# Performance work log

Measured on AMD Instinct MI355X. Metric: run time of the kernel, lower is better.

Reference implementation:

```python
import jax, jax.numpy as jnp
import numpy as np

NEG = -1e30  # stand-in for -inf on the H-attention diagonal (matches INF helper)


def _conv1x1(w, b, x):
    # w: [O, C], x: [B, C, H, W]
    return jnp.einsum('oc,bchw->bohw', w, x) + b[None, :, None, None]


def _cc_attn(q, k, v):
    """Criss-cross attention: q,k [B,Cq,H,W], v [B,C,H,W] -> [B,C,H,W]."""
    B, _, H, W = q.shape
    # column (H) energies: query at (h,w) attends to keys at (h', w)
    eH = jnp.einsum('bchw,bcjw->bhwj', q, k)  # [B,H,W,H]
    eye = jnp.eye(H, dtype=bool)[None, :, None, :]
    eH = jnp.where(eye, NEG, eH)  # mask h==h' (self counted once via W pass)
    # row (W) energies: query at (h,w) attends to keys at (h, w')
    eW = jnp.einsum('bchw,bchj->bhwj', q, k)  # [B,H,W,W]
    att = jax.nn.softmax(jnp.concatenate([eH, eW], axis=3), axis=3)  # [B,H,W,H+W]
    aH, aW = att[..., :H], att[..., H:]
    outH = jnp.einsum('bhwj,bcjw->bchw', aH, v)
    outW = jnp.einsum('bhwj,bchj->bchw', aW, v)
    return outH + outW


def setup_inputs() -> dict:
    key = jax.random.key(0)
    ks = jax.random.split(key, 14)
    B, C, H, W = 8, 256, 96, 96
    Cq = C // 8
    n = jax.random.normal
    return {
        'x': n(ks[0], (B, C, H, W), jnp.float32),
        'y': n(ks[1], (B, C, H, W), jnp.float32),
        'Wq': n(ks[2], (Cq, C), jnp.float32) * 0.05,
        'bq': n(ks[3], (Cq,), jnp.float32) * 0.05,
        'Wk': n(ks[4], (Cq, C), jnp.float32) * 0.05,
        'bk': n(ks[5], (Cq,), jnp.float32) * 0.05,
        'Wv': n(ks[6], (C, C), jnp.float32) * 0.05,
        'bv': n(ks[7], (C,), jnp.float32) * 0.05,
        'gamma1': n(ks[8], (1,), jnp.float32) * 0.1,
        'gamma2': n(ks[9], (1,), jnp.float32) * 0.1,
        'Wd': n(ks[10], (2 * C, 1, 3, 3), jnp.float32) * 0.1,  # depthwise, groups=2C
        'bd': n(ks[11], (2 * C,), jnp.float32) * 0.05,
        'Wp': n(ks[12], (C, 2 * C), jnp.float32) * 0.05,  # pointwise 1x1
        'bp': n(ks[13], (C,), jnp.float32) * 0.05,
    }


def reference(x, y, Wq, bq, Wk, bk, Wv, bv, gamma1, gamma2, Wd, bd, Wp, bp):
    qx = _conv1x1(Wq, bq, x)
    kx = _conv1x1(Wk, bk, x)
    vx = _conv1x1(Wv, bv, x)
    qy = _conv1x1(Wq, bq, y)
    ky = _conv1x1(Wk, bk, y)
    vy = _conv1x1(Wv, bv, y)
    # pass 1: attention weights from x, values from y
    out1 = gamma1[0] * _cc_attn(qx, kx, vy) + x
    # pass 2: attention weights from y, values from x
    out2 = gamma2[0] * _cc_attn(qy, ky, vx) + y
    z = jnp.concatenate([out1, out2], axis=1)  # [B, 2C, H, W]
    # depthwise 3x3 (groups = 2C), padding 1
    z = jax.lax.conv_general_dilated(
        z, Wd, window_strides=(1, 1), padding='SAME',
        feature_group_count=z.shape[1],
        dimension_numbers=('NCHW', 'OIHW', 'NCHW')) + bd[None, :, None, None]
    # pointwise 1x1 then LeakyReLU (torch default negative_slope=0.01)
    z = _conv1x1(Wp, bp, z)
    return jax.nn.leaky_relu(z, negative_slope=0.01)
```

## Files before the change

### kernel.cpp

```cpp
#include <hip/hip_runtime.h>
#include <hip/hip_bf16.h>

constexpr int kB  = 8;
constexpr int kC  = 256;
constexpr int kCq = 32;
constexpr int kH  = 96;
constexpr int kW  = 96;
constexpr int kP  = kH * kW;

using bf16x8 = __attribute__((ext_vector_type(8))) short;
using bf16x4 = __attribute__((ext_vector_type(4))) short;
using f32x4  = __attribute__((ext_vector_type(4))) float;

__device__ inline bf16x8 ld_lds8(const __hip_bfloat16* p) {
    bf16x4 lo = *(const bf16x4*)p;
    bf16x4 hi = *(const bf16x4*)(p + 4);
    return __builtin_shufflevector(lo, hi, 0, 1, 2, 3, 4, 5, 6, 7);
}

__device__ inline void async_copy16(const void* g, void* l) {
    __builtin_amdgcn_global_load_lds(
        (const __attribute__((address_space(1))) unsigned int*)g,
        (__attribute__((address_space(3))) unsigned int*)l, 16, 0, 0);
}

__global__ __launch_bounds__(256) void w_convert(
    const float* __restrict__ Wq, const float* __restrict__ Wk,
    const float* __restrict__ Wv,
    __hip_bfloat16* __restrict__ Wqkb, __hip_bfloat16* __restrict__ Wvb)
{
    const int i = blockIdx.x * 256 + threadIdx.x;
    if (i < 8192)       Wqkb[i] = __float2bfloat16(Wq[i]);
    else if (i < 16384) Wqkb[i] = __float2bfloat16(Wk[i - 8192]);
    else                Wvb[i - 16384] = __float2bfloat16(Wv[i - 16384]);
}

__global__ __launch_bounds__(256, 2) void qkv_mfma(
    const float* __restrict__ in_qk, const float* __restrict__ in_v,
    const __hip_bfloat16* __restrict__ Wqkb, const __hip_bfloat16* __restrict__ Wvb,
    const float* __restrict__ bq, const float* __restrict__ bk,
    const float* __restrict__ bv,
    __hip_bfloat16* __restrict__ Qbh, __hip_bfloat16* __restrict__ Qbl,
    __hip_bfloat16* __restrict__ Kbh, __hip_bfloat16* __restrict__ Kbl,
    __hip_bfloat16* __restrict__ Vpm, __hip_bfloat16* __restrict__ Vhw)
{
    __shared__ __align__(16) char smem[34816];
    float* stg = (float*)smem;
    __hip_bfloat16* vt = (__hip_bfloat16*)smem;

    const int b = blockIdx.y, t = threadIdx.x;
    const int wv = t >> 6, l = t & 63;
    const int n = l & 15, q = l >> 4;
    const int p0 = blockIdx.x * 64;
    const int p  = p0 + wv * 16 + n;
    const size_t bP = (size_t)b * kP;

    const float* __restrict__ xq = in_qk + (size_t)b * kC * kP + p0;
    const float* __restrict__ xv = in_v  + (size_t)b * kC * kP + p0;

    f32x4 acc[20];
#pragma unroll
    for (int i = 0; i < 20; i++) acc[i] = (f32x4)0.f;

    const int lrow = l >> 4, lpx = (l & 15) * 4;
#define STAGE_CHUNK(kc, buf)                                                   \
    {                                                                          \
        const size_t cb = (size_t)(kc) * 32;                                   \
        float* dq = stg + (size_t)(buf) * 4096;                                \
        float* dv = dq + 2048;                                                 \
        _Pragma("unroll")                                                      \
        for (int j = 0; j < 2; j++) {                                          \
            const int r0 = wv * 8 + j * 4;                                     \
            async_copy16(&xq[(cb + r0 + lrow) * kP + lpx], &dq[r0 * 64]);      \
            async_copy16(&xv[(cb + r0 + lrow) * kP + lpx], &dv[r0 * 64]);      \
        }                                                                      \
    }

    STAGE_CHUNK(0, 0);
    __syncthreads();

    int cur = 0;
    for (int kc = 0; kc < 8; kc++) {
        if (kc < 7) STAGE_CHUNK(kc + 1, cur ^ 1);

        const int c0 = kc * 32 + q * 8;

        bf16x8 wq[4], wv2[16];
#pragma unroll
        for (int mt = 0; mt < 4; mt++)
            wq[mt] = *(const bf16x8*)(Wqkb + ((mt * 16 + n) << 8) + c0);
#pragma unroll
        for (int mt = 0; mt < 16; mt++)
            wv2[mt] = *(const bf16x8*)(Wvb + ((mt * 16 + n) << 8) + c0);

        const float* __restrict__ sqf = stg + (size_t)cur * 4096;
        const float* __restrict__ svf = sqf + 2048;
        const int pl = wv * 16 + n;
        union { bf16x8 v; __hip_bfloat16 h[8]; } bfq, bfv;
#pragma unroll
        for (int j = 0; j < 8; j++)
            bfq.h[j] = __float2bfloat16(sqf[(q * 8 + j) * 64 + pl]);
#pragma unroll
        for (int j = 0; j < 8; j++)
            bfv.h[j] = __float2bfloat16(svf[(q * 8 + j) * 64 + pl]);

#pragma unroll
        for (int mt = 0; mt < 4; mt++)
            acc[mt] = __builtin_amdgcn_mfma_f32_16x16x32_bf16(wq[mt], bfq.v, acc[mt], 0, 0, 0);
#pragma unroll
        for (int mt = 0; mt < 16; mt++)
            acc[4 + mt] = __builtin_amdgcn_mfma_f32_16x16x32_bf16(wv2[mt], bfv.v, acc[4 + mt], 0, 0, 0);

        __syncthreads();
        cur ^= 1;
    }
#undef STAGE_CHUNK

#pragma unroll
    for (int mt = 0; mt < 2; mt++) {
        float4 bias = *(const float4*)&bq[mt * 16 + q * 4];
        float vv[4] = { acc[mt][0] + bias.x, acc[mt][1] + bias.y,
                        acc[mt][2] + bias.z, acc[mt][3] + bias.w };
        union { ushort4 u; __hip_bfloat16 h[4]; } hi, lo;
#pragma unroll
        for (int r = 0; r < 4; r++) {
            __hip_bfloat16 h = __float2bfloat16(vv[r]);
            hi.h[r] = h;
            lo.h[r] = __float2bfloat16(vv[r] - __bfloat162float(h));
        }
        *(ushort4*)&Qbh[(bP + p) * kCq + mt * 16 + q * 4] = hi.u;
        *(ushort4*)&Qbl[(bP + p) * kCq + mt * 16 + q * 4] = lo.u;
    }
#pragma unroll
    for (int mt = 2; mt < 4; mt++) {
        float4 bias = *(const float4*)&bk[(mt - 2) * 16 + q * 4];
        float vv[4] = { acc[mt][0] + bias.x, acc[mt][1] + bias.y,
                        acc[mt][2] + bias.z, acc[mt][3] + bias.w };
        union { ushort4 u; __hip_bfloat16 h[4]; } hi, lo;
#pragma unroll
        for (int r = 0; r < 4; r++) {
            __hip_bfloat16 h = __float2bfloat16(vv[r]);
            hi.h[r] = h;
            lo.h[r] = __float2bfloat16(vv[r] - __bfloat162float(h));
        }
        *(ushort4*)&Kbh[(bP + p) * kCq + (mt - 2) * 16 + q * 4] = hi.u;
        *(ushort4*)&Kbl[(bP + p) * kCq + (mt - 2) * 16 + q * 4] = lo.u;
    }

#pragma unroll
    for (int mt = 0; mt < 16; mt++) {
        float4 bias = *(const float4*)&bv[mt * 16 + q * 4];
        float vv[4] = { acc[4 + mt][0] + bias.x, acc[4 + mt][1] + bias.y,
                        acc[4 + mt][2] + bias.z, acc[4 + mt][3] + bias.w };
        union { ushort4 u; __hip_bfloat16 h[4]; } pm;
#pragma unroll
        for (int r = 0; r < 4; r++) pm.h[r] = __float2bfloat16(vv[r]);
        *(ushort4*)&Vpm[(bP + p) * kC + mt * 16 + q * 4] = pm.u;
#pragma unroll
        for (int r = 0; r < 4; r++)
            vt[(mt * 16 + q * 4 + r) * 68 + wv * 16 + n] = pm.h[r];
    }
    __syncthreads();

    {
        __hip_bfloat16* dst = Vhw + ((size_t)b * kC + t) * kP + p0;
#pragma unroll
        for (int j = 0; j < 8; j++) {
            bf16x8 row = ld_lds8(&vt[t * 68 + j * 8]);
            *(bf16x8*)&dst[j * 8] = row;
        }
    }
}

__global__ __launch_bounds__(256) void cc_stats(
    const __hip_bfloat16* __restrict__ Qbh, const __hip_bfloat16* __restrict__ Qbl,
    const __hip_bfloat16* __restrict__ Kbh, const __hip_bfloat16* __restrict__ Kbl,
    float* __restrict__ Sm, float* __restrict__ Si)
{
    __shared__ __align__(16) __hip_bfloat16 QH[96][36], QLo[96][36];
    __shared__ __align__(16) __hip_bfloat16 KH[96][36], KLo[96][36];
    __shared__ __align__(16) float EL[96][97];
    const int w = blockIdx.x, b = blockIdx.y;
    const int t = threadIdx.x;
    const size_t bP = (size_t)b * kP;

    for (int idx = t; idx < 768; idx += 256) {
        int row = idx >> 3, ch = (idx & 7) * 4;
        size_t g = (bP + (size_t)row * kW + w) * kCq + ch;
        *(ushort4*)&QH[row][ch]  = *(const ushort4*)&Qbh[g];
        *(ushort4*)&QLo[row][ch] = *(const ushort4*)&Qbl[g];
        *(ushort4*)&KH[row][ch]  = *(const ushort4*)&Kbh[g];
        *(ushort4*)&KLo[row][ch] = *(const ushort4*)&Kbl[g];
    }
    __syncthreads();

    const int wv = t >> 6, l = t & 63, ln = l & 15, lq = l >> 4;
#pragma unroll
    for (int s = 0; s < 9; s++) {
        int tile = wv * 9 + s, it = tile / 6, jt = tile % 6;
        bf16x8 ah = ld_lds8(&QH[it * 16 + ln][lq * 8]);
        bf16x8 al = ld_lds8(&QLo[it * 16 + ln][lq * 8]);
        bf16x8 bh = ld_lds8(&KH[jt * 16 + ln][lq * 8]);
        bf16x8 bl = ld_lds8(&KLo[jt * 16 + ln][lq * 8]);
        f32x4 d = (f32x4)0.f;
        d = __builtin_amdgcn_mfma_f32_16x16x32_bf16(al, bh, d, 0, 0, 0);
        d = __builtin_amdgcn_mfma_f32_16x16x32_bf16(ah, bl, d, 0, 0, 0);
        d = __builtin_amdgcn_mfma_f32_16x16x32_bf16(ah, bh, d, 0, 0, 0);
#pragma unroll
        for (int r = 0; r < 4; r++)
            EL[it * 16 + lq * 4 + r][jt * 16 + ln] = d[r];
    }
    __syncthreads();

    const int sub = t & 7;
    for (int pi = t >> 3; pi < 96; pi += 32) {
        float ev[12];
        float mx = -3.0e38f;
#pragma unroll
        for (int k = 0; k < 12; k++) {
            int j = sub + 8 * k;
            float e = EL[pi][j];
            if (j == pi) e = -3.0e38f;
            ev[k] = e;
            mx = fmaxf(mx, e);
        }
#pragma unroll
        for (int k = 1; k < 8; k <<= 1) mx = fmaxf(mx, __shfl_xor(mx, k, 8));
        float ss = 0.f;
#pragma unroll
        for (int k = 0; k < 12; k++) ss += __expf(ev[k] - mx);
#pragma unroll
        for (int k = 1; k < 8; k <<= 1) ss += __shfl_xor(ss, k, 8);
        if (sub == 0) {
            Sm[bP + (size_t)pi * kW + w] = mx;
            Si[bP + (size_t)pi * kW + w] = ss;
        }
    }
}

__global__ __launch_bounds__(256) void cc_pass1(
    const __hip_bfloat16* __restrict__ Qbh, const __hip_bfloat16* __restrict__ Qbl,
    const __hip_bfloat16* __restrict__ Kbh, const __hip_bfloat16* __restrict__ Kbl,
    const __hip_bfloat16* __restrict__ Vhw,
    const float* __restrict__ res_in, const float* __restrict__ gamma_p,
    __hip_bfloat16* __restrict__ Zb, float* __restrict__ Sm, float* __restrict__ Si,
    int s_off)
{
    __shared__ __align__(16) __hip_bfloat16 QH[32][36], QLo[32][36];
    __shared__ __align__(16) __hip_bfloat16 KH[96][36], KLo[96][36];
    __shared__ __align__(16) float EL[32][97];
    __shared__ __align__(16) __hip_bfloat16 attL[32][100];
    const int wt = blockIdx.x, h = blockIdx.y, b = blockIdx.z;
    const int w0 = wt * 32;
    const int t = threadIdx.x;
    const size_t bP = (size_t)b * kP;

    {
        int row = t >> 3, ch = (t & 7) * 4;
        size_t g = (bP + (size_t)h * kW + w0 + row) * kCq + ch;
        *(ushort4*)&QH[row][ch]  = *(const ushort4*)&Qbh[g];
        *(ushort4*)&QLo[row][ch] = *(const ushort4*)&Qbl[g];
    }
    for (int idx = t; idx < 768; idx += 256) {
        int row = idx >> 3, ch = (idx & 7) * 4;
        size_t g = (bP + (size_t)h * kW + row) * kCq + ch;
        *(ushort4*)&KH[row][ch]  = *(const ushort4*)&Kbh[g];
        *(ushort4*)&KLo[row][ch] = *(const ushort4*)&Kbl[g];
    }
    __syncthreads();

    const int wv = t >> 6, l = t & 63, ln = l & 15, lq = l >> 4;
#pragma unroll
    for (int s = 0; s < 3; s++) {
        int tile = wv * 3 + s, it = tile / 6, jt = tile % 6;
        bf16x8 ah = ld_lds8(&QH[it * 16 + ln][lq * 8]);
        bf16x8 al = ld_lds8(&QLo[it * 16 + ln][lq * 8]);
        bf16x8 bh = ld_lds8(&KH[jt * 16 + ln][lq * 8]);
        bf16x8 bl = ld_lds8(&KLo[jt * 16 + ln][lq * 8]);
        f32x4 d = (f32x4)0.f;
        d = __builtin_amdgcn_mfma_f32_16x16x32_bf16(al, bh, d, 0, 0, 0);
        d = __builtin_amdgcn_mfma_f32_16x16x32_bf16(ah, bl, d, 0, 0, 0);
        d = __builtin_amdgcn_mfma_f32_16x16x32_bf16(ah, bh, d, 0, 0, 0);
#pragma unroll
        for (int r = 0; r < 4; r++)
            EL[it * 16 + lq * 4 + r][jt * 16 + ln] = d[r];
    }
    __syncthreads();

    {
        const int pi = t >> 3, sub = t & 7;
        size_t sidx = bP + (size_t)h * kW + w0 + pi;
        float mH = Sm[sidx], sH = Si[sidx];
        float ev[12];
        float mx = mH;
#pragma unroll
        for (int k = 0; k < 12; k++) {
            float e = EL[pi][sub + 8 * k];
            ev[k] = e;
            mx = fmaxf(mx, e);
        }
#pragma unroll
        for (int k = 1; k < 8; k <<= 1) mx = fmaxf(mx, __shfl_xor(mx, k, 8));
        float ss = 0.f;
#pragma unroll
        for (int k = 0; k < 12; k++) { float e = __expf(ev[k] - mx); ev[k] = e; ss += e; }
#pragma unroll
        for (int k = 1; k < 8; k <<= 1) ss += __shfl_xor(ss, k, 8);
        float stot = ss + sH * __expf(mH - mx);
        float inv = 1.0f / stot;
        if (sub == 0) { Sm[sidx] = mx; Si[sidx] = inv; }
#pragma unroll
        for (int k = 0; k < 12; k++)
            attL[pi][sub + 8 * k] = __float2bfloat16(ev[k] * inv);
    }
    __syncthreads();

    const float* __restrict__ res = res_in + (size_t)b * kC * kP + (size_t)h * kW + w0;
    float4 rsv[4][2];
#pragma unroll
    for (int c4 = 0; c4 < 4; c4++) {
        const int c = (wv * 4 + c4) * 16 + ln;
#pragma unroll
        for (int it = 0; it < 2; it++)
            rsv[c4][it] = *(const float4*)&res[(size_t)c * kP + it * 16 + lq * 4];
    }

    bf16x8 aF[2][3];
#pragma unroll
    for (int it = 0; it < 2; it++)
#pragma unroll
        for (int j3 = 0; j3 < 3; j3++)
            aF[it][j3] = ld_lds8(&attL[it * 16 + ln][j3 * 32 + lq * 8]);

    f32x4 acc[2][4];
#pragma unroll
    for (int it = 0; it < 2; it++)
#pragma unroll
        for (int c4 = 0; c4 < 4; c4++) acc[it][c4] = (f32x4)0.f;

#pragma unroll
    for (int c4 = 0; c4 < 4; c4++) {
        const int c = (wv * 4 + c4) * 16 + ln;
        const __hip_bfloat16* vr = Vhw + ((size_t)b * kC + c) * kP + (size_t)h * kW;
        bf16x8 bF0 = *(const bf16x8*)&vr[lq * 8];
        bf16x8 bF1 = *(const bf16x8*)&vr[32 + lq * 8];
        bf16x8 bF2 = *(const bf16x8*)&vr[64 + lq * 8];
#pragma unroll
        for (int it = 0; it < 2; it++) {
            acc[it][c4] = __builtin_amdgcn_mfma_f32_16x16x32_bf16(aF[it][0], bF0, acc[it][c4], 0, 0, 0);
            acc[it][c4] = __builtin_amdgcn_mfma_f32_16x16x32_bf16(aF[it][1], bF1, acc[it][c4], 0, 0, 0);
            acc[it][c4] = __builtin_amdgcn_mfma_f32_16x16x32_bf16(aF[it][2], bF2, acc[it][c4], 0, 0, 0);
        }
    }

    const float gamma = gamma_p[0];
#pragma unroll
    for (int c4 = 0; c4 < 4; c4++) {
        const int c = (wv * 4 + c4) * 16 + ln;
#pragma unroll
        for (int it = 0; it < 2; it++) {
            const float* rp = (const float*)&rsv[c4][it];
#pragma unroll
            for (int r = 0; r < 4; r++) {
                int i = it * 16 + lq * 4 + r;
                float z = gamma * acc[it][c4][r] + rp[r];
                Zb[(bP + (size_t)h * kW + w0 + i) * 512 + s_off + c] = __float2bfloat16(z);
            }
        }
    }
}

__global__ __launch_bounds__(256) void cc_pass2(
    const __hip_bfloat16* __restrict__ Qbh, const __hip_bfloat16* __restrict__ Qbl,
    const __hip_bfloat16* __restrict__ Kbh, const __hip_bfloat16* __restrict__ Kbl,
    const __hip_bfloat16* __restrict__ Vpm,
    const float* __restrict__ gamma_p, __hip_bfloat16* __restrict__ Zb,
    const float* __restrict__ Sm, const float* __restrict__ Si, int s_off)
{
    __shared__ __align__(16) __hip_bfloat16 QH[32][36], QLo[32][36];
    __shared__ __align__(16) __hip_bfloat16 KH[96][36], KLo[96][36];
    __shared__ __align__(16) __hip_bfloat16 VL[96][260];
    __shared__ __align__(16) __hip_bfloat16 attL[32][100];
    const int ht = blockIdx.x, w = blockIdx.y, b = blockIdx.z;
    const int h0 = ht * 32;
    const int t = threadIdx.x;
    const size_t bP = (size_t)b * kP;

    {
        int row = t >> 3, ch = (t & 7) * 4;
        size_t g = (bP + (size_t)(h0 + row) * kW + w) * kCq + ch;
        *(ushort4*)&QH[row][ch]  = *(const ushort4*)&Qbh[g];
        *(ushort4*)&QLo[row][ch] = *(const ushort4*)&Qbl[g];
    }
    for (int idx = t; idx < 768; idx += 256) {
        int row = idx >> 3, ch = (idx & 7) * 4;
        size_t g = (bP + (size_t)row * kW + w) * kCq + ch;
        *(ushort4*)&KH[row][ch]  = *(const ushort4*)&Kbh[g];
        *(ushort4*)&KLo[row][ch] = *(const ushort4*)&Kbl[g];
    }
    for (int idx = t; idx < 96 * 32; idx += 256) {
        int j = idx >> 5, cg = (idx & 31) * 8;
        const ushort4* src = (const ushort4*)&Vpm[(bP + (size_t)j * kW + w) * kC + cg];
        ushort4 v0 = src[0], v1 = src[1];
        *(ushort4*)&VL[j][cg]     = v0;
        *(ushort4*)&VL[j][cg + 4] = v1;
    }
    __syncthreads();

    const int wv = t >> 6, l = t & 63, ln = l & 15, lq = l >> 4;
#pragma unroll
    for (int s = 0; s < 3; s++) {
        int tile = wv * 3 + s, it = tile / 6, jt = tile % 6;
        bf16x8 ah = ld_lds8(&QH[it * 16 + ln][lq * 8]);
        bf16x8 al = ld_lds8(&QLo[it * 16 + ln][lq * 8]);
        bf16x8 bh = ld_lds8(&KH[jt * 16 + ln][lq * 8]);
        bf16x8 bl = ld_lds8(&KLo[jt * 16 + ln][lq * 8]);
        f32x4 d = (f32x4)0.f;
        d = __builtin_amdgcn_mfma_f32_16x16x32_bf16(al, bh, d, 0, 0, 0);
        d = __builtin_amdgcn_mfma_f32_16x16x32_bf16(ah, bl, d, 0, 0, 0);
        d = __builtin_amdgcn_mfma_f32_16x16x32_bf16(ah, bh, d, 0, 0, 0);
        const int j = jt * 16 + ln;
#pragma unroll
        for (int r = 0; r < 4; r++) {
            int i = it * 16 + lq * 4 + r;
            size_t sidx = bP + (size_t)(h0 + i) * kW + w;
            float m = Sm[sidx], inv = Si[sidx];
            float a = (j == h0 + i) ? 0.f : __expf(d[r] - m) * inv;
            attL[i][j] = __float2bfloat16(a);
        }
    }
    __syncthreads();

    bf16x8 aF[2][3];
#pragma unroll
    for (int it = 0; it < 2; it++)
#pragma unroll
        for (int j3 = 0; j3 < 3; j3++)
            aF[it][j3] = ld_lds8(&attL[it * 16 + ln][j3 * 32 + lq * 8]);

    f32x4 acc[2][4];
#pragma unroll
    for (int it = 0; it < 2; it++)
#pragma unroll
        for (int c4 = 0; c4 < 4; c4++) acc[it][c4] = (f32x4)0.f;

#pragma unroll
    for (int c4 = 0; c4 < 4; c4++) {
        const int c = (wv * 4 + c4) * 16 + ln;
#pragma unroll
        for (int j3 = 0; j3 < 3; j3++) {
            union { bf16x8 v; __hip_bfloat16 h[8]; } bF;
#pragma unroll
            for (int jj = 0; jj < 8; jj++)
                bF.h[jj] = VL[j3 * 32 + lq * 8 + jj][c];
#pragma unroll
            for (int it = 0; it < 2; it++)
                acc[it][c4] = __builtin_amdgcn_mfma_f32_16x16x32_bf16(aF[it][j3], bF.v, acc[it][c4], 0, 0, 0);
        }
    }

    const float gamma = gamma_p[0];
#pragma unroll
    for (int c4 = 0; c4 < 4; c4++) {
        const int c = (wv * 4 + c4) * 16 + ln;
#pragma unroll
        for (int it = 0; it < 2; it++) {
#pragma unroll
            for (int r = 0; r < 4; r++) {
                int i = it * 16 + lq * 4 + r;
                size_t zi = (bP + (size_t)(h0 + i) * kW + w) * 512 + s_off + c;
                float old = __bfloat162float(Zb[zi]);
                Zb[zi] = __float2bfloat16(old + gamma * acc[it][c4][r]);
            }
        }
    }
}

__global__ __launch_bounds__(256) void wp_convert(
    const float* __restrict__ Wp, __hip_bfloat16* __restrict__ Wpb)
{
    const int i = blockIdx.x * 256 + threadIdx.x;
    Wpb[i] = __float2bfloat16(Wp[i]);
}

__global__ __launch_bounds__(256, 4) void dwpw(
    const __hip_bfloat16* __restrict__ Zb,
    const float* __restrict__ Wdw, const float* __restrict__ bd,
    const __hip_bfloat16* __restrict__ Wpb, const float* __restrict__ bp,
    float* __restrict__ out)
{
    __shared__ __align__(16) __hip_bfloat16 zs[16][520];

    const int wt = blockIdx.x, h = blockIdx.y, b = blockIdx.z;
    const int w0 = wt * 16;
    const int t = threadIdx.x;
    const size_t bP = (size_t)b * kP;

    const int l = t & 63, wv = t >> 6;
    const int lo16 = l & 15, q = l >> 4;

    const bf16x8* __restrict__ Bb[4];
#pragma unroll
    for (int nt = 0; nt < 4; nt++)
        Bb[nt] = (const bf16x8*)(Wpb + (size_t)(wv * 64 + nt * 16 + lo16) * 512);

    {
        float wd0[9], wd1[9];
#pragma unroll
        for (int k = 0; k < 9; k++) {
            wd0[k] = Wdw[(size_t)(2 * t) * 9 + k];
            wd1[k] = Wdw[(size_t)(2 * t + 1) * 9 + k];
        }
        const float b0 = bd[2 * t], b1 = bd[2 * t + 1];
        const uint* __restrict__ Zp = (const uint*)Zb + bP * 256 + t;
        const bool rvm = (h > 0), rvp = (h < kH - 1);

#pragma unroll
        for (int j0 = 0; j0 < 16; j0 += 8) {
            uint raw[10][3];
#pragma unroll
            for (int col = 0; col < 10; col++) {
                const int ww = w0 + j0 - 1 + col;
                const bool cv = (ww >= 0) && (ww < kW);
#pragma unroll
                for (int r = 0; r < 3; r++) {
                    const bool v = cv && (r == 1 || (r == 0 ? rvm : rvp));
                    raw[col][r] = v ? Zp[(size_t)((h + r - 1) * kW + ww) * 256] : 0u;
                }
            }
            float2 wfc[10][3];
#pragma unroll
            for (int col = 0; col < 10; col++)
#pragma unroll
                for (int r = 0; r < 3; r++) {
                    __hip_bfloat162 z2 = *(const __hip_bfloat162*)&raw[col][r];
                    wfc[col][r] = __bfloat1622float2(z2);
                }
#pragma unroll
            for (int j = 0; j < 8; j++) {
                float a0 = b0, a1 = b1;
#pragma unroll
                for (int r = 0; r < 3; r++) {
#pragma unroll
                    for (int dw = 0; dw < 3; dw++) {
                        const float2 z = wfc[j + dw][r];
                        const int k = r * 3 + dw;
                        a0 += wd0[k] * z.x;
                        a1 += wd1[k] * z.y;
                    }
                }
                __hip_bfloat162 pz;
                pz.x = __float2bfloat16(a0);
                pz.y = __float2bfloat16(a1);
                ((__hip_bfloat162*)&zs[j0 + j][0])[t] = pz;
            }
        }
    }

    bf16x8 wbuf[4][4];
#pragma unroll
    for (int kp = 0; kp < 4; kp++)
#pragma unroll
        for (int nt = 0; nt < 4; nt++)
            wbuf[kp][nt] = Bb[nt][kp * 4 + q];

    __syncthreads();

    f32x4 acc[4];
#pragma unroll
    for (int nt = 0; nt < 4; nt++) acc[nt] = (f32x4)0.f;

#pragma unroll
    for (int kc = 0; kc < 16; kc++) {
        const int s = kc & 3;
        bf16x8 a0 = ld_lds8(&zs[lo16][kc * 32 + q * 8]);
        bf16x8 wcur[4];
#pragma unroll
        for (int nt = 0; nt < 4; nt++) wcur[nt] = wbuf[s][nt];
        if (kc < 12) {
#pragma unroll
            for (int nt = 0; nt < 4; nt++)
                wbuf[s][nt] = Bb[nt][(kc + 4) * 4 + q];
        }
#pragma unroll
        for (int nt = 0; nt < 4; nt++)
            acc[nt] = __builtin_amdgcn_mfma_f32_16x16x32_bf16(a0, wcur[nt], acc[nt], 0, 0, 0);
    }

#pragma unroll
    for (int nt = 0; nt < 4; nt++) {
        const int ol = wv * 64 + nt * 16 + lo16;
        const float bias = bp[ol];
        float4 rv;
        float v0 = acc[nt][0] + bias; rv.x = v0 > 0.f ? v0 : 0.01f * v0;
        float v1 = acc[nt][1] + bias; rv.y = v1 > 0.f ? v1 : 0.01f * v1;
        float v2 = acc[nt][2] + bias; rv.z = v2 > 0.f ? v2 : 0.01f * v2;
        float v3 = acc[nt][3] + bias; rv.w = v3 > 0.f ? v3 : 0.01f * v3;
        *(float4*)&out[((size_t)b * 256 + ol) * kP + (size_t)h * kW + w0 + q * 4] = rv;
    }
}

extern "C" void kernel_launch(void* const* d_in, const int* in_sizes, int n_in,
                              void* d_out, int out_size, void* d_ws, size_t ws_size,
                              hipStream_t stream)
{
    const float* x   = (const float*)d_in[0];
    const float* y   = (const float*)d_in[1];
    const float* Wq  = (const float*)d_in[2];
    const float* bq  = (const float*)d_in[3];
    const float* Wk  = (const float*)d_in[4];
    const float* bk  = (const float*)d_in[5];
    const float* Wv  = (const float*)d_in[6];
    const float* bv  = (const float*)d_in[7];
    const float* g1  = (const float*)d_in[8];
    const float* g2  = (const float*)d_in[9];
    const float* Wdw = (const float*)d_in[10];
    const float* bd  = (const float*)d_in[11];
    const float* Wp  = (const float*)d_in[12];
    const float* bp  = (const float*)d_in[13];
    float* out = (float*)d_out;

    char* wsb = (char*)d_ws;
    __hip_bfloat16* Zb  = (__hip_bfloat16*)wsb;
    __hip_bfloat16* Qbh = (__hip_bfloat16*)(wsb + 75497472);
    __hip_bfloat16* Qbl = Qbh + 2359296;
    __hip_bfloat16* Kbh = (__hip_bfloat16*)(wsb + 84934656);
    __hip_bfloat16* Kbl = Kbh + 2359296;
    float* Sm = (float*)(wsb + 94371840);
    float* Si = (float*)(wsb + 94666752);
    __hip_bfloat16* Wqkb = (__hip_bfloat16*)Sm;
    __hip_bfloat16* Wvb  = ((__hip_bfloat16*)Sm) + 16384;
    __hip_bfloat16* Wpb  = (__hip_bfloat16*)(wsb + 75497472);
    __hip_bfloat16* Vpm  = (__hip_bfloat16*)d_out;
    __hip_bfloat16* Vhw  = Vpm + 18874368;

    hipLaunchKernelGGL(w_convert, dim3(320), dim3(256), 0, stream,
                       Wq, Wk, Wv, Wqkb, Wvb);
    hipLaunchKernelGGL(qkv_mfma, dim3(kP / 64, kB), dim3(256), 0, stream,
                       x, y, Wqkb, Wvb, bq, bk, bv, Qbh, Qbl, Kbh, Kbl, Vpm, Vhw);
    hipLaunchKernelGGL(cc_stats, dim3(kW, kB), dim3(256), 0, stream,
                       Qbh, Qbl, Kbh, Kbl, Sm, Si);
    hipLaunchKernelGGL(cc_pass1, dim3(kW / 32, kH, kB), dim3(256), 0, stream,
                       Qbh, Qbl, Kbh, Kbl, Vhw, x, g1, Zb, Sm, Si, 0);
    hipLaunchKernelGGL(cc_pass2, dim3(kH / 32, kW, kB), dim3(256), 0, stream,
                       Qbh, Qbl, Kbh, Kbl, Vpm, g1, Zb, Sm, Si, 0);
    hipLaunchKernelGGL(w_convert, dim3(320), dim3(256), 0, stream,
                       Wq, Wk, Wv, Wqkb, Wvb);
    hipLaunchKernelGGL(qkv_mfma, dim3(kP / 64, kB), dim3(256), 0, stream,
                       y, x, Wqkb, Wvb, bq, bk, bv, Qbh, Qbl, Kbh, Kbl, Vpm, Vhw);
    hipLaunchKernelGGL(cc_stats, dim3(kW, kB), dim3(256), 0, stream,
                       Qbh, Qbl, Kbh, Kbl, Sm, Si);
    hipLaunchKernelGGL(cc_pass1, dim3(kW / 32, kH, kB), dim3(256), 0, stream,
                       Qbh, Qbl, Kbh, Kbl, Vhw, y, g2, Zb, Sm, Si, 256);
    hipLaunchKernelGGL(cc_pass2, dim3(kH / 32, kW, kB), dim3(256), 0, stream,
                       Qbh, Qbl, Kbh, Kbl, Vpm, g2, Zb, Sm, Si, 256);
    hipLaunchKernelGGL(wp_convert, dim3(512), dim3(256), 0, stream, Wp, Wpb);
    hipLaunchKernelGGL(dwpw, dim3(kW / 16, kH, kB), dim3(256), 0, stream,
                       Zb, Wdw, bd, Wpb, bp, out);
}
```

Measured before the change: 816.3 us.

## Replace pixel-major V with column-transposed V layout for H-pass attention

Stops qkv_mfma from writing the pixel-major V copy and adds a small transpose kernel that builds a per-channel, column-major (w,h) copy of V from the existing [C,H,W] copy. cc_pass2 then loads its MFMA B-operands directly from global memory as contiguous 8-element vectors instead of staging a 96x256 V tile in LDS and gathering it with scalar strided reads. This removes a large LDS allocation and its fill loop, which may raise occupancy. In exchange it adds an extra kernel launch and a full read and write of V per pass.

```diff
diff --git a/kernel.cpp b/kernel.cpp
--- a/kernel.cpp
+++ b/kernel.cpp
@@ -42,7 +42,7 @@
     const float* __restrict__ bv,
     __hip_bfloat16* __restrict__ Qbh, __hip_bfloat16* __restrict__ Qbl,
     __hip_bfloat16* __restrict__ Kbh, __hip_bfloat16* __restrict__ Kbl,
-    __hip_bfloat16* __restrict__ Vpm, __hip_bfloat16* __restrict__ Vhw)
+    __hip_bfloat16* __restrict__ Vhw)
 {
     __shared__ __align__(16) char smem[34816];
     float* stg = (float*)smem;
@@ -152,13 +152,9 @@
         float4 bias = *(const float4*)&bv[mt * 16 + q * 4];
         float vv[4] = { acc[4 + mt][0] + bias.x, acc[4 + mt][1] + bias.y,
                         acc[4 + mt][2] + bias.z, acc[4 + mt][3] + bias.w };
-        union { ushort4 u; __hip_bfloat16 h[4]; } pm;
-#pragma unroll
-        for (int r = 0; r < 4; r++) pm.h[r] = __float2bfloat16(vv[r]);
-        *(ushort4*)&Vpm[(bP + p) * kC + mt * 16 + q * 4] = pm.u;
 #pragma unroll
         for (int r = 0; r < 4; r++)
-            vt[(mt * 16 + q * 4 + r) * 68 + wv * 16 + n] = pm.h[r];
+            vt[(mt * 16 + q * 4 + r) * 68 + wv * 16 + n] = __float2bfloat16(vv[r]);
     }
     __syncthreads();
 
@@ -169,6 +165,31 @@
             bf16x8 row = ld_lds8(&vt[t * 68 + j * 8]);
             *(bf16x8*)&dst[j * 8] = row;
         }
+    }
+}
+
+__global__ __launch_bounds__(256) void vcol_tr(
+    const __hip_bfloat16* __restrict__ Vhw, __hip_bfloat16* __restrict__ Vcol)
+{
+    __shared__ __hip_bfloat16 tile[96][105];
+    const int bc = blockIdx.x;
+    const size_t base = (size_t)bc * kP;
+    const int t = threadIdx.x;
+
+    for (int ci = t; ci < 1152; ci += 256) {
+        const int off = ci * 8, h = off / 96, w = off - h * 96;
+        union { bf16x8 v; __hip_bfloat16 e[8]; } in;
+        in.v = *(const bf16x8*)&Vhw[base + off];
+#pragma unroll
+        for (int j = 0; j < 8; j++) tile[h][w + j] = in.e[j];
+    }
+    __syncthreads();
+    for (int ci = t; ci < 1152; ci += 256) {
+        const int off = ci * 8, w = off / 96, h = off - w * 96;
+        union { bf16x8 v; __hip_bfloat16 e[8]; } o;
+#pragma unroll
+        for (int j = 0; j < 8; j++) o.e[j] = tile[h + j][w];
+        *(bf16x8*)&Vcol[base + off] = o.v;
     }
 }
 
@@ -373,13 +394,12 @@
 __global__ __launch_bounds__(256) void cc_pass2(
     const __hip_bfloat16* __restrict__ Qbh, const __hip_bfloat16* __restrict__ Qbl,
     const __hip_bfloat16* __restrict__ Kbh, const __hip_bfloat16* __restrict__ Kbl,
-    const __hip_bfloat16* __restrict__ Vpm,
+    const __hip_bfloat16* __restrict__ Vcol,
     const float* __restrict__ gamma_p, __hip_bfloat16* __restrict__ Zb,
     const float* __restrict__ Sm, const float* __restrict__ Si, int s_off)
 {
     __shared__ __align__(16) __hip_bfloat16 QH[32][36], QLo[32][36];
     __shared__ __align__(16) __hip_bfloat16 KH[96][36], KLo[96][36];
-    __shared__ __align__(16) __hip_bfloat16 VL[96][260];
     __shared__ __align__(16) __hip_bfloat16 attL[32][100];
     const int ht = blockIdx.x, w = blockIdx.y, b = blockIdx.z;
     const int h0 = ht * 32;
@@ -397,13 +417,6 @@
         size_t g = (bP + (size_t)row * kW + w) * kCq + ch;
         *(ushort4*)&KH[row][ch]  = *(const ushort4*)&Kbh[g];
         *(ushort4*)&KLo[row][ch] = *(const ushort4*)&Kbl[g];
-    }
-    for (int idx = t; idx < 96 * 32; idx += 256) {
-        int j = idx >> 5, cg = (idx & 31) * 8;
-        const ushort4* src = (const ushort4*)&Vpm[(bP + (size_t)j * kW + w) * kC + cg];
-        ushort4 v0 = src[0], v1 = src[1];
-        *(ushort4*)&VL[j][cg]     = v0;
-        *(ushort4*)&VL[j][cg + 4] = v1;
     }
     __syncthreads();
 
@@ -447,15 +460,15 @@
 #pragma unroll
     for (int c4 = 0; c4 < 4; c4++) {
         const int c = (wv * 4 + c4) * 16 + ln;
-#pragma unroll
-        for (int j3 = 0; j3 < 3; j3++) {
-            union { bf16x8 v; __hip_bfloat16 h[8]; } bF;
-#pragma unroll
-            for (int jj = 0; jj < 8; jj++)
-                bF.h[jj] = VL[j3 * 32 + lq * 8 + jj][c];
-#pragma unroll
-            for (int it = 0; it < 2; it++)
-                acc[it][c4] = __builtin_amdgcn_mfma_f32_16x16x32_bf16(aF[it][j3], bF.v, acc[it][c4], 0, 0, 0);
+        const __hip_bfloat16* vc = Vcol + ((size_t)b * kC + c) * kP + (size_t)w * kH;
+        bf16x8 bF0 = *(const bf16x8*)&vc[lq * 8];
+        bf16x8 bF1 = *(const bf16x8*)&vc[32 + lq * 8];
+        bf16x8 bF2 = *(const bf16x8*)&vc[64 + lq * 8];
+#pragma unroll
+        for (int it = 0; it < 2; it++) {
+            acc[it][c4] = __builtin_amdgcn_mfma_f32_16x16x32_bf16(aF[it][0], bF0, acc[it][c4], 0, 0, 0);
+            acc[it][c4] = __builtin_amdgcn_mfma_f32_16x16x32_bf16(aF[it][1], bF1, acc[it][c4], 0, 0, 0);
+            acc[it][c4] = __builtin_amdgcn_mfma_f32_16x16x32_bf16(aF[it][2], bF2, acc[it][c4], 0, 0, 0);
         }
     }
 
@@ -631,29 +644,31 @@
     __hip_bfloat16* Wqkb = (__hip_bfloat16*)Sm;
     __hip_bfloat16* Wvb  = ((__hip_bfloat16*)Sm) + 16384;
     __hip_bfloat16* Wpb  = (__hip_bfloat16*)(wsb + 75497472);
-    __hip_bfloat16* Vpm  = (__hip_bfloat16*)d_out;
-    __hip_bfloat16* Vhw  = Vpm + 18874368;
+    __hip_bfloat16* Vcol = (__hip_bfloat16*)d_out;
+    __hip_bfloat16* Vhw  = Vcol + 18874368;
 
     hipLaunchKernelGGL(w_convert, dim3(320), dim3(256), 0, stream,
                        Wq, Wk, Wv, Wqkb, Wvb);
     hipLaunchKernelGGL(qkv_mfma, dim3(kP / 64, kB), dim3(256), 0, stream,
-                       x, y, Wqkb, Wvb, bq, bk, bv, Qbh, Qbl, Kbh, Kbl, Vpm, Vhw);
+                       x, y, Wqkb, Wvb, bq, bk, bv, Qbh, Qbl, Kbh, Kbl, Vhw);
+    hipLaunchKernelGGL(vcol_tr, dim3(kB * kC), dim3(256), 0, stream, Vhw, Vcol);
     hipLaunchKernelGGL(cc_stats, dim3(kW, kB), dim3(256), 0, stream,
                        Qbh, Qbl, Kbh, Kbl, Sm, Si);
     hipLaunchKernelGGL(cc_pass1, dim3(kW / 32, kH, kB), dim3(256), 0, stream,
                        Qbh, Qbl, Kbh, Kbl, Vhw, x, g1, Zb, Sm, Si, 0);
     hipLaunchKernelGGL(cc_pass2, dim3(kH / 32, kW, kB), dim3(256), 0, stream,
-                       Qbh, Qbl, Kbh, Kbl, Vpm, g1, Zb, Sm, Si, 0);
+                       Qbh, Qbl, Kbh, Kbl, Vcol, g1, Zb, Sm, Si, 0);
     hipLaunchKernelGGL(w_convert, dim3(320), dim3(256), 0, stream,
                        Wq, Wk, Wv, Wqkb, Wvb);
     hipLaunchKernelGGL(qkv_mfma, dim3(kP / 64, kB), dim3(256), 0, stream,
-                       y, x, Wqkb, Wvb, bq, bk, bv, Qbh, Qbl, Kbh, Kbl, Vpm, Vhw);
+                       y, x, Wqkb, Wvb, bq, bk, bv, Qbh, Qbl, Kbh, Kbl, Vhw);
+    hipLaunchKernelGGL(vcol_tr, dim3(kB * kC), dim3(256), 0, stream, Vhw, Vcol);
     hipLaunchKernelGGL(cc_stats, dim3(kW, kB), dim3(256), 0, stream,
                        Qbh, Qbl, Kbh, Kbl, Sm, Si);
     hipLaunchKernelGGL(cc_pass1, dim3(kW / 32, kH, kB), dim3(256), 0, stream,
                        Qbh, Qbl, Kbh, Kbl, Vhw, y, g2, Zb, Sm, Si, 256);
     hipLaunchKernelGGL(cc_pass2, dim3(kH / 32, kW, kB), dim3(256), 0, stream,
-                       Qbh, Qbl, Kbh, Kbl, Vpm, g2, Zb, Sm, Si, 256);
+                       Qbh, Qbl, Kbh, Kbl, Vcol, g2, Zb, Sm, Si, 256);
     hipLaunchKernelGGL(wp_convert, dim3(512), dim3(256), 0, stream, Wp, Wpb);
     hipLaunchKernelGGL(dwpw, dim3(kW / 16, kH, kB), dim3(256), 0, stream,
                        Zb, Wdw, bd, Wpb, bp, out);
```

Measured after the change: 821.8 us. No clear change (+0.7%).

## Store Z in channel-octet blocked layout and vectorize depthwise conv loads

Applied to the files above, without the earlier changes.

Changes the intermediate Z buffer from pixel-major with 512 channels to a blocked layout of [B][64 octets][pixels][8 channels]. The pass1 and pass2 writers now scatter into this layout. The depthwise stage reads 16-byte vectors of 8 channels per pixel, with clamped addresses and masking, and takes transposed depthwise weights staged in LDS. The aim is fewer, wider and better-coalesced loads in dwpw, at the cost of more scattered 2-byte stores in the attention passes and an extra small weight-transpose kernel.

```diff
diff --git a/kernel.cpp b/kernel.cpp
--- a/kernel.cpp
+++ b/kernel.cpp
@@ -11,6 +11,10 @@
 using bf16x8 = __attribute__((ext_vector_type(8))) short;
 using bf16x4 = __attribute__((ext_vector_type(4))) short;
 using f32x4  = __attribute__((ext_vector_type(4))) float;
+
+__device__ inline size_t zb_idx(int b, int cglob, int px) {
+    return (((size_t)b * 64 + (cglob >> 3)) * kP + px) * 8 + (cglob & 7);
+}
 
 __device__ inline bf16x8 ld_lds8(const __hip_bfloat16* p) {
     bf16x4 lo = *(const bf16x4*)p;
@@ -364,7 +368,7 @@
             for (int r = 0; r < 4; r++) {
                 int i = it * 16 + lq * 4 + r;
                 float z = gamma * acc[it][c4][r] + rp[r];
-                Zb[(bP + (size_t)h * kW + w0 + i) * 512 + s_off + c] = __float2bfloat16(z);
+                Zb[zb_idx(b, s_off + c, h * kW + w0 + i)] = __float2bfloat16(z);
             }
         }
     }
@@ -468,7 +472,7 @@
 #pragma unroll
             for (int r = 0; r < 4; r++) {
                 int i = it * 16 + lq * 4 + r;
-                size_t zi = (bP + (size_t)(h0 + i) * kW + w) * 512 + s_off + c;
+                size_t zi = zb_idx(b, s_off + c, (h0 + i) * kW + w);
                 float old = __bfloat162float(Zb[zi]);
                 Zb[zi] = __float2bfloat16(old + gamma * acc[it][c4][r]);
             }
@@ -483,79 +487,96 @@
     Wpb[i] = __float2bfloat16(Wp[i]);
 }
 
+__global__ __launch_bounds__(256) void wdw_convert(
+    const float* __restrict__ Wdw, float* __restrict__ Wdwt)
+{
+    const int i = blockIdx.x * 256 + threadIdx.x;
+    if (i < 9 * 512) {
+        const int k = i / 512, c = i - k * 512;
+        Wdwt[i] = Wdw[(size_t)c * 9 + k];
+    }
+}
+
 __global__ __launch_bounds__(256, 4) void dwpw(
     const __hip_bfloat16* __restrict__ Zb,
-    const float* __restrict__ Wdw, const float* __restrict__ bd,
+    const float* __restrict__ Wdwt, const float* __restrict__ bd,
     const __hip_bfloat16* __restrict__ Wpb, const float* __restrict__ bp,
     float* __restrict__ out)
 {
+    __shared__ __align__(16) float wdl[9][512];
     __shared__ __align__(16) __hip_bfloat16 zs[16][520];
 
     const int wt = blockIdx.x, h = blockIdx.y, b = blockIdx.z;
     const int w0 = wt * 16;
     const int t = threadIdx.x;
-    const size_t bP = (size_t)b * kP;
 
     const int l = t & 63, wv = t >> 6;
     const int lo16 = l & 15, q = l >> 4;
 
+    for (int i = t; i < 9 * 512; i += 256)
+        ((float*)wdl)[i] = Wdwt[i];
+    __syncthreads();
+
+    {
+        const int px16 = t & 15, og = t >> 4;
+        const bool rvm = (h > 0), rvp = (h < kH - 1);
+
+        for (int cg = 0; cg < 4; cg++) {
+            const int oct = cg * 16 + og;
+            const int ch0 = oct * 8;
+            const __hip_bfloat16* __restrict__ Zo =
+                Zb + ((size_t)b * 64 + oct) * (size_t)kP * 8;
+
+            bf16x8 raw[9];
+            bool val[9];
+#pragma unroll
+            for (int r = 0; r < 3; r++) {
+                const int hh = h + r - 1;
+                const int hcl = hh < 0 ? 0 : (hh > kH - 1 ? kH - 1 : hh);
+                const bool hv = (r == 1) || (r == 0 ? rvm : rvp);
+#pragma unroll
+                for (int dw = 0; dw < 3; dw++) {
+                    const int ww = w0 + px16 + dw - 1;
+                    const int wcl = ww < 0 ? 0 : (ww > kW - 1 ? kW - 1 : ww);
+                    raw[r * 3 + dw] =
+                        *(const bf16x8*)&Zo[(size_t)(hcl * kW + wcl) * 8];
+                    val[r * 3 + dw] = hv && (ww >= 0) && (ww < kW);
+                }
+            }
+
+            float4 bA = *(const float4*)&bd[ch0];
+            float4 bB = *(const float4*)&bd[ch0 + 4];
+            float a[8] = { bA.x, bA.y, bA.z, bA.w, bB.x, bB.y, bB.z, bB.w };
+
+#pragma unroll
+            for (int k = 0; k < 9; k++) {
+                union { bf16x8 v; __hip_bfloat162 h2[4]; } u;
+                u.v = raw[k];
+                float4 wA = *(const float4*)&wdl[k][ch0];
+                float4 wB = *(const float4*)&wdl[k][ch0 + 4];
+                float wk[8] = { wA.x, wA.y, wA.z, wA.w, wB.x, wB.y, wB.z, wB.w };
+                const bool v = val[k];
+#pragma unroll
+                for (int jj = 0; jj < 4; jj++) {
+                    float2 f = __bfloat1622float2(u.h2[jj]);
+                    f.x = v ? f.x : 0.f;
+                    f.y = v ? f.y : 0.f;
+                    a[2 * jj]     += wk[2 * jj]     * f.x;
+                    a[2 * jj + 1] += wk[2 * jj + 1] * f.y;
+                }
+            }
+
+            union { bf16x8 v; __hip_bfloat16 h8[8]; } o;
+#pragma unroll
+            for (int j = 0; j < 8; j++) o.h8[j] = __float2bfloat16(a[j]);
+            *(bf16x8*)&zs[px16][ch0] = o.v;
+        }
+    }
+
     const bf16x8* __restrict__ Bb[4];
 #pragma unroll
     for (int nt = 0; nt < 4; nt++)
         Bb[nt] = (const bf16x8*)(Wpb + (size_t)(wv * 64 + nt * 16 + lo16) * 512);
-
-    {
-        float wd0[9], wd1[9];
-#pragma unroll
-        for (int k = 0; k < 9; k++) {
-            wd0[k] = Wdw[(size_t)(2 * t) * 9 + k];
-            wd1[k] = Wdw[(size_t)(2 * t + 1) * 9 + k];
-        }
-        const float b0 = bd[2 * t], b1 = bd[2 * t + 1];
-        const uint* __restrict__ Zp = (const uint*)Zb + bP * 256 + t;
-        const bool rvm = (h > 0), rvp = (h < kH - 1);
-
-#pragma unroll
-        for (int j0 = 0; j0 < 16; j0 += 8) {
-            uint raw[10][3];
-#pragma unroll
-            for (int col = 0; col < 10; col++) {
-                const int ww = w0 + j0 - 1 + col;
-                const bool cv = (ww >= 0) && (ww < kW);
-#pragma unroll
-                for (int r = 0; r < 3; r++) {
-                    const bool v = cv && (r == 1 || (r == 0 ? rvm : rvp));
-                    raw[col][r] = v ? Zp[(size_t)((h + r - 1) * kW + ww) * 256] : 0u;
-                }
-            }
-            float2 wfc[10][3];
-#pragma unroll
-            for (int col = 0; col < 10; col++)
-#pragma unroll
-                for (int r = 0; r < 3; r++) {
-                    __hip_bfloat162 z2 = *(const __hip_bfloat162*)&raw[col][r];
-                    wfc[col][r] = __bfloat1622float2(z2);
-                }
-#pragma unroll
-            for (int j = 0; j < 8; j++) {
-                float a0 = b0, a1 = b1;
-#pragma unroll
-                for (int r = 0; r < 3; r++) {
-#pragma unroll
-                    for (int dw = 0; dw < 3; dw++) {
-                        const float2 z = wfc[j + dw][r];
-                        const int k = r * 3 + dw;
-                        a0 += wd0[k] * z.x;
-                        a1 += wd1[k] * z.y;
-                    }
-                }
-                __hip_bfloat162 pz;
-                pz.x = __float2bfloat16(a0);
-                pz.y = __float2bfloat16(a1);
-                ((__hip_bfloat162*)&zs[j0 + j][0])[t] = pz;
-            }
-        }
-    }
 
     bf16x8 wbuf[4][4];
 #pragma unroll
@@ -631,6 +652,7 @@
     __hip_bfloat16* Wqkb = (__hip_bfloat16*)Sm;
     __hip_bfloat16* Wvb  = ((__hip_bfloat16*)Sm) + 16384;
     __hip_bfloat16* Wpb  = (__hip_bfloat16*)(wsb + 75497472);
+    float* Wdwt = (float*)(wsb + 84934656);
     __hip_bfloat16* Vpm  = (__hip_bfloat16*)d_out;
     __hip_bfloat16* Vhw  = Vpm + 18874368;
 
@@ -655,6 +677,7 @@
     hipLaunchKernelGGL(cc_pass2, dim3(kH / 32, kW, kB), dim3(256), 0, stream,
                        Qbh, Qbl, Kbh, Kbl, Vpm, g2, Zb, Sm, Si, 256);
     hipLaunchKernelGGL(wp_convert, dim3(512), dim3(256), 0, stream, Wp, Wpb);
+    hipLaunchKernelGGL(wdw_convert, dim3(18), dim3(256), 0, stream, Wdw, Wdwt);
     hipLaunchKernelGGL(dwpw, dim3(kW / 16, kH, kB), dim3(256), 0, stream,
-                       Zb, Wdw, bd, Wpb, bp, out);
-}
+                       Zb, Wdwt, bd, Wpb, bp, out);
+}
```

Result: slower. 977.6 us (+19.8%).
